# Optimization experiments

Measured on AMD Instinct MI355X. Metric: run time of the kernel, lower is better.

## Reference

```python
import jax, jax.numpy as jnp
import numpy as np

B = 128
N_ATOMS = 4096
NB, NA, NT = 4095, 4094, 4093
MAX_LEN = 5 * NT  # 20465, longest packed column (torsions)
EPS = 1e-8


def setup_inputs() -> dict:
    key = jax.random.key(0)
    ks = jax.random.split(key, 24)
    feats = jnp.zeros((B, MAX_LEN, 9), jnp.float32)
    # col 0: atom type ids
    atoms = jax.random.randint(ks[0], (B, N_ATOMS), 0, 6)
    # col 5: coords, flattened (N_ATOMS, 3)
    coords = jax.random.normal(ks[1], (B, N_ATOMS, 3), jnp.float32) * 5.0
    # col 6: bonds (i, j, type)
    bonds = jnp.stack([
        jax.random.randint(ks[2], (B, NB), 0, N_ATOMS),
        jax.random.randint(ks[3], (B, NB), 0, N_ATOMS),
        jax.random.randint(ks[4], (B, NB), 0, 15)], axis=-1)
    # col 7: angles (i, j, k, type)
    angles = jnp.stack([
        jax.random.randint(ks[5], (B, NA), 0, N_ATOMS),
        jax.random.randint(ks[6], (B, NA), 0, N_ATOMS),
        jax.random.randint(ks[7], (B, NA), 0, N_ATOMS),
        jax.random.randint(ks[8], (B, NA), 0, 13)], axis=-1)
    # col 8: torsions (i, j, k, l, type)
    tors = jnp.stack([
        jax.random.randint(ks[9], (B, NT), 0, N_ATOMS),
        jax.random.randint(ks[10], (B, NT), 0, N_ATOMS),
        jax.random.randint(ks[11], (B, NT), 0, N_ATOMS),
        jax.random.randint(ks[12], (B, NT), 0, N_ATOMS),
        jax.random.randint(ks[13], (B, NT), 0, 25)], axis=-1)
    feats = feats.at[:, :N_ATOMS, 0].set(atoms.astype(jnp.float32))
    feats = feats.at[:, :3 * N_ATOMS, 5].set(coords.reshape(B, -1))
    feats = feats.at[:, :3 * NB, 6].set(bonds.reshape(B, -1).astype(jnp.float32))
    feats = feats.at[:, :4 * NA, 7].set(angles.reshape(B, -1).astype(jnp.float32))
    feats = feats.at[:, :5 * NT, 8].set(tors.reshape(B, -1).astype(jnp.float32))
    lengths = jnp.tile(jnp.array(
        [[N_ATOMS, 0, 0, 0, 0, 3 * N_ATOMS, 3 * NB, 4 * NA, 5 * NT]],
        jnp.int32), (B, 1))
    bond_type = jnp.stack([jnp.ones(15), jax.random.uniform(ks[14], (15,), minval=1.0, maxval=2.0)], -1).astype(jnp.float32)
    angle_type = jnp.stack([jnp.ones(13), jax.random.uniform(ks[15], (13,), minval=1.0, maxval=3.0)], -1).astype(jnp.float32)
    tor_type = jnp.stack([jnp.ones(25), jax.random.uniform(ks[16], (25,), minval=0.0, maxval=3.14)], -1).astype(jnp.float32)
    multiplicity = jax.random.randint(ks[17], (25,), 1, 4)
    opt_pars = jax.random.uniform(ks[18], (47,), minval=0.5, maxval=1.5).astype(jnp.float32)
    return {"features": feats, "lengths": lengths, "bond_type": bond_type,
            "angle_type": angle_type, "tor_type": tor_type,
            "multiplicity": multiplicity, "opt_pars": opt_pars}


def _sample_energy(f, bond_type, angle_type, tor_type, multiplicity, opt_pars):
    coords = f[:3 * N_ATOMS, 5].reshape(-1, 3)                      # [N,3]
    bonds = f[:3 * NB, 6].astype(jnp.int32).reshape(-1, 3)          # [NB,3]
    angles = f[:4 * NA, 7].astype(jnp.int32).reshape(-1, 4)         # [NA,4]
    tors = f[:5 * NT, 8].astype(jnp.int32).reshape(-1, 5)           # [NT,5]

    # bonds: harmonic k*(r - r0)^2
    d = coords[bonds[:, 0]] - coords[bonds[:, 1]]
    r = jnp.sqrt(jnp.sum(d * d, -1) + EPS)
    pb = bond_type[bonds[:, 2]]
    e_bond = opt_pars[0] * jnp.sum(pb[:, 0] * (r - pb[:, 1]) ** 2)

    # angles: harmonic k*(theta - theta0)^2
    v1 = coords[angles[:, 0]] - coords[angles[:, 1]]
    v2 = coords[angles[:, 2]] - coords[angles[:, 1]]
    cosang = jnp.sum(v1 * v2, -1) / (
        jnp.sqrt(jnp.sum(v1 * v1, -1) + EPS) * jnp.sqrt(jnp.sum(v2 * v2, -1) + EPS))
    theta = jnp.arccos(jnp.clip(cosang, -1.0 + 1e-6, 1.0 - 1e-6))
    pa = angle_type[angles[:, 3]]
    e_ang = opt_pars[1] * jnp.sum(pa[:, 0] * (theta - pa[:, 1]) ** 2)

    # torsions: periodic k*(1 + cos(n*phi - delta))
    ci, cj, ck, cl = (coords[tors[:, m]] for m in range(4))
    b1, b2, b3 = cj - ci, ck - cj, cl - ck
    n1 = jnp.cross(b1, b2)
    n2 = jnp.cross(b2, b3)
    b2n = b2 / jnp.sqrt(jnp.sum(b2 * b2, -1, keepdims=True) + EPS)
    m1 = jnp.cross(n1, b2n)
    phi = jnp.arctan2(jnp.sum(m1 * n2, -1), jnp.sum(n1 * n2, -1))
    pt = tor_type[tors[:, 4]]
    n_mult = multiplicity[tors[:, 4]].astype(jnp.float32)
    e_tor = opt_pars[2] * jnp.sum(pt[:, 0] * (1.0 + jnp.cos(n_mult * phi - pt[:, 1])))

    return jnp.stack([e_bond, e_ang, e_tor])


def reference(features, lengths, bond_type, angle_type, tor_type, multiplicity, opt_pars):
    # lengths are uniform across batch (constants above); vmap over batch dim
    return jax.vmap(_sample_energy, in_axes=(0, None, None, None, None, None))(
        features, bond_type, angle_type, tor_type, multiplicity, opt_pars)
```

## Files before the change

kernel.cpp:

```cpp
#include <hip/hip_runtime.h>
#include <math.h>

#define BATCH      128
#define N_ATOMS    4096
#define NB         4095
#define NA         4094
#define NT         4093
#define FSTRIDE    184185
#define COORD_SPAN 110592
#define TOTAL_F4   5893920u
#define EPSV       1e-8f
#define THREADS    1024
#define WAVES      16
#define TILE_F     1080
#define NTILES     171
#define CTILES     103
#define SCR_F4     272

#define WAVE_LDS_FENCE()  do { asm volatile("" ::: "memory"); \
                               __builtin_amdgcn_wave_barrier(); } while (0)

__global__ __launch_bounds__(THREADS, 1) void
local_energy_fused(const float* __restrict__ F,
                   const float* __restrict__ bond_type,
                   const float* __restrict__ angle_type,
                   const float* __restrict__ tor_type,
                   const int*   __restrict__ multiplicity,
                   const float* __restrict__ opt_pars,
                   float*       __restrict__ out)
{
    __shared__ float scx[N_ATOMS];
    __shared__ float scy[N_ATOMS];
    __shared__ float scz[N_ATOMS];
    __shared__ __align__(16) float4 scr[WAVES][SCR_F4];
    __shared__ float sbt[30], sat[26], stt[50], smu[25];
    __shared__ float sred[WAVES * 3];

    const int b   = blockIdx.x;
    const int x   = b & 7;
    const int g   = b >> 3;
    const int s   = (g & 15) * 8 + x;
    const int p   = g >> 4;
    const int tid = threadIdx.x;
    const int w   = tid >> 6;
    const int l   = tid & 63;
    const size_t sbase = (size_t)s * FSTRIDE;
    const int d = (int)(sbase & 3);
    const float4* __restrict__ F4 = (const float4*)F;

    if (tid < 30)                      sbt[tid]       = bond_type[tid];
    else if (tid >= 32 && tid < 58)    sat[tid - 32]  = angle_type[tid - 32];
    else if (tid >= 64 && tid < 114)   stt[tid - 64]  = tor_type[tid - 64];
    else if (tid >= 128 && tid < 153)  smu[tid - 128] = (float)multiplicity[tid - 128];

    float* const swf = (float*)scr[w];

    {
        float4 cur[5];
        int t = w;
        {
            const size_t q0 = (sbase + (size_t)t * TILE_F) >> 2;
            const int nf = (COORD_SPAN - t * TILE_F < TILE_F) ? COORD_SPAN - t * TILE_F : TILE_F;
            const int nq = (d + nf + 3) >> 2;
            #pragma unroll
            for (int i = 0; i < 5; ++i) {
                const int k = l + 64 * i;
                cur[i] = (k < nq && q0 + k < TOTAL_F4) ? F4[q0 + k]
                                                       : make_float4(0.f, 0.f, 0.f, 0.f);
            }
        }
        for (; t < CTILES; t += WAVES) {
            const int tn = t + WAVES;
            float4 nxt[5];
            #pragma unroll
            for (int i = 0; i < 5; ++i) nxt[i] = make_float4(0.f, 0.f, 0.f, 0.f);
            if (tn < CTILES) {
                const size_t q0 = (sbase + (size_t)tn * TILE_F) >> 2;
                const int nf = (COORD_SPAN - tn * TILE_F < TILE_F) ? COORD_SPAN - tn * TILE_F : TILE_F;
                const int nq = (d + nf + 3) >> 2;
                #pragma unroll
                for (int i = 0; i < 5; ++i) {
                    const int k = l + 64 * i;
                    if (k < nq && q0 + k < TOTAL_F4) nxt[i] = F4[q0 + k];
                }
            }
            #pragma unroll
            for (int i = 0; i < 4; ++i) scr[w][l + 64 * i] = cur[i];
            if (l < 15) scr[w][l + 256] = cur[4];
            WAVE_LDS_FENCE();

            const int na = (N_ATOMS - 40 * t < 40) ? N_ATOMS - 40 * t : 40;
            if (l < na) {
                const int base = d + 27 * l;
                const int atom = 40 * t + l;
                scx[atom] = swf[base + 5];
                scy[atom] = swf[base + 14];
                scz[atom] = swf[base + 23];
            }
            WAVE_LDS_FENCE();
            #pragma unroll
            for (int i = 0; i < 5; ++i) cur[i] = nxt[i];
        }
    }
    __syncthreads();

    float e_bond = 0.f, e_ang = 0.f, e_tor = 0.f;
    {
        const int tlo = (p == 0) ? 0  : 86;
        const int thi = (p == 0) ? 86 : NTILES;
        float4 cur[5];
        int t = tlo + w;
        if (t < thi) {
            const size_t q0 = (sbase + (size_t)t * TILE_F) >> 2;
            const int nf = (FSTRIDE - t * TILE_F < TILE_F) ? FSTRIDE - t * TILE_F : TILE_F;
            const int nq = (d + nf + 3) >> 2;
            #pragma unroll
            for (int i = 0; i < 5; ++i) {
                const int k = l + 64 * i;
                cur[i] = (k < nq && q0 + k < TOTAL_F4) ? F4[q0 + k]
                                                       : make_float4(0.f, 0.f, 0.f, 0.f);
            }
        }
        for (; t < thi; t += WAVES) {
            const int tn = t + WAVES;
            float4 nxt[5];
            #pragma unroll
            for (int i = 0; i < 5; ++i) nxt[i] = make_float4(0.f, 0.f, 0.f, 0.f);
            if (tn < thi) {
                const size_t q0 = (sbase + (size_t)tn * TILE_F) >> 2;
                const int nf = (FSTRIDE - tn * TILE_F < TILE_F) ? FSTRIDE - tn * TILE_F : TILE_F;
                const int nq = (d + nf + 3) >> 2;
                #pragma unroll
                for (int i = 0; i < 5; ++i) {
                    const int k = l + 64 * i;
                    if (k < nq && q0 + k < TOTAL_F4) nxt[i] = F4[q0 + k];
                }
            }
            #pragma unroll
            for (int i = 0; i < 4; ++i) scr[w][l + 64 * i] = cur[i];
            if (l < 15) scr[w][l + 256] = cur[4];
            WAVE_LDS_FENCE();

            int nb = NB - 40 * t; nb = (nb > 40) ? 40 : nb;
            if (l < nb) {
                const int base = d + 27 * l;
                const int a0 = (int)swf[base + 6];
                const int a1 = (int)swf[base + 15];
                const int bt = (int)swf[base + 24];
                const float dx = scx[a0] - scx[a1];
                const float dy = scy[a0] - scy[a1];
                const float dz = scz[a0] - scz[a1];
                const float r  = sqrtf(dx*dx + dy*dy + dz*dz + EPSV);
                const float t0 = r - sbt[bt * 2 + 1];
                e_bond += sbt[bt * 2 + 0] * t0 * t0;
            }

            int na = NA - 30 * t; na = (na > 30) ? 30 : na;
            if (l < na) {
                const int base = d + 36 * l;
                const int a0 = (int)swf[base + 7];
                const int a1 = (int)swf[base + 16];
                const int a2 = (int)swf[base + 25];
                const int at = (int)swf[base + 34];
                const float v1x = scx[a0] - scx[a1];
                const float v1y = scy[a0] - scy[a1];
                const float v1z = scz[a0] - scz[a1];
                const float v2x = scx[a2] - scx[a1];
                const float v2y = scy[a2] - scy[a1];
                const float v2z = scz[a2] - scz[a1];
                const float d12 = v1x*v2x + v1y*v2y + v1z*v2z;
                const float n1  = sqrtf(v1x*v1x + v1y*v1y + v1z*v1z + EPSV);
                const float n2  = sqrtf(v2x*v2x + v2y*v2y + v2z*v2z + EPSV);
                float cosang = d12 / (n1 * n2);
                cosang = fminf(fmaxf(cosang, -1.0f + 1e-6f), 1.0f - 1e-6f);
                const float t0 = acosf(cosang) - sat[at * 2 + 1];
                e_ang += sat[at * 2 + 0] * t0 * t0;
            }

            int ntr = NT - 24 * t; ntr = (ntr > 24) ? 24 : ntr;
            if (l < ntr) {
                const int base = d + 45 * l;
                const int ai = (int)swf[base + 8];
                const int aj = (int)swf[base + 17];
                const int ak = (int)swf[base + 26];
                const int al = (int)swf[base + 35];
                const int tt = (int)swf[base + 44];

                const float b1x = scx[aj] - scx[ai], b1y = scy[aj] - scy[ai], b1z = scz[aj] - scz[ai];
                const float b2x = scx[ak] - scx[aj], b2y = scy[ak] - scy[aj], b2z = scz[ak] - scz[aj];
                const float b3x = scx[al] - scx[ak], b3y = scy[al] - scy[ak], b3z = scz[al] - scz[ak];

                const float n1x = b1y*b2z - b1z*b2y;
                const float n1y = b1z*b2x - b1x*b2z;
                const float n1z = b1x*b2y - b1y*b2x;
                const float n2x = b2y*b3z - b2z*b3y;
                const float n2y = b2z*b3x - b2x*b3z;
                const float n2z = b2x*b3y - b2y*b3x;

                const float inv = 1.0f / sqrtf(b2x*b2x + b2y*b2y + b2z*b2z + EPSV);
                const float bnx = b2x * inv, bny = b2y * inv, bnz = b2z * inv;

                const float m1x = n1y*bnz - n1z*bny;
                const float m1y = n1z*bnx - n1x*bnz;
                const float m1z = n1x*bny - n1y*bnx;

                const float sy = m1x*n2x + m1y*n2y + m1z*n2z;
                const float sx = n1x*n2x + n1y*n2y + n1z*n2z;
                const float phi = atan2f(sy, sx);

                e_tor += stt[tt * 2 + 0] * (1.0f + cosf(smu[tt] * phi - stt[tt * 2 + 1]));
            }

            WAVE_LDS_FENCE();
            #pragma unroll
            for (int i = 0; i < 5; ++i) cur[i] = nxt[i];
        }
    }

    for (int off = 32; off > 0; off >>= 1) {
        e_bond += __shfl_down(e_bond, off);
        e_ang  += __shfl_down(e_ang,  off);
        e_tor  += __shfl_down(e_tor,  off);
    }
    if (l == 0) {
        sred[w * 3 + 0] = e_bond;
        sred[w * 3 + 1] = e_ang;
        sred[w * 3 + 2] = e_tor;
    }
    __syncthreads();
    if (tid == 0) {
        float eb = 0.f, ea = 0.f, et = 0.f;
        for (int i = 0; i < WAVES; ++i) {
            eb += sred[i * 3 + 0];
            ea += sred[i * 3 + 1];
            et += sred[i * 3 + 2];
        }
        atomicAdd(&out[s * 3 + 0], opt_pars[0] * eb);
        atomicAdd(&out[s * 3 + 1], opt_pars[1] * ea);
        atomicAdd(&out[s * 3 + 2], opt_pars[2] * et);
    }
}

extern "C" void kernel_launch(void* const* d_in, const int* in_sizes, int n_in,
                              void* d_out, int out_size, void* d_ws, size_t ws_size,
                              hipStream_t stream) {
    const float* F            = (const float*)d_in[0];
    const float* bond_type    = (const float*)d_in[2];
    const float* angle_type   = (const float*)d_in[3];
    const float* tor_type     = (const float*)d_in[4];
    const int*   multiplicity = (const int*)  d_in[5];
    const float* opt_pars     = (const float*)d_in[6];
    float* out = (float*)d_out;

    hipMemsetAsync(out, 0, (size_t)out_size * sizeof(float), stream);

    local_energy_fused<<<dim3(BATCH * 2), dim3(THREADS), 0, stream>>>(
        F, bond_type, angle_type, tor_type, multiplicity, opt_pars, out);
}
```

Baseline: 158.3 us.

## Stash bond/angle/torsion indices in LDS during coord pass to balance work

During the coordinate-loading pass (tiles 0-102), each block now also decodes the bond, angle and torsion index records in its half of that range into compact ushort arrays in LDS. It evaluates them afterwards with all threads in flat strided loops. The second streaming pass now covers only tiles 103-170, which hold the remaining angles and torsions. This avoids re-reading tiles that are already in cache, splits the work evenly across the two blocks per sample, and removes bounds checks. In exchange it uses more LDS and adds a second compute phase whose gathers may have more bank conflicts.

```diff
diff --git a/kernel.cpp b/kernel.cpp
--- a/kernel.cpp
+++ b/kernel.cpp
@@ -7,14 +7,13 @@
 #define NA         4094
 #define NT         4093
 #define FSTRIDE    184185
-#define COORD_SPAN 110592
 #define TOTAL_F4   5893920u
 #define EPSV       1e-8f
 #define THREADS    1024
 #define WAVES      16
 #define TILE_F     1080
 #define NTILES     171
-#define CTILES     103
+#define ATILES     103
 #define SCR_F4     272
 
 #define WAVE_LDS_FENCE()  do { asm volatile("" ::: "memory"); \
@@ -33,6 +32,9 @@
     __shared__ float scy[N_ATOMS];
     __shared__ float scz[N_ATOMS];
     __shared__ __align__(16) float4 scr[WAVES][SCR_F4];
+    __shared__ unsigned short sbB[2080 * 3];
+    __shared__ unsigned short sbA[1560 * 4];
+    __shared__ unsigned short sbT[1248 * 5];
     __shared__ float sbt[30], sat[26], stt[50], smu[25];
     __shared__ float sred[WAVES * 3];
 
@@ -55,33 +57,35 @@
 
     float* const swf = (float*)scr[w];
 
+    const int Alo = p ? 51 : 0;
+    const int Ahi = p ? 103 : 51;
+    const int cnt_b = p ? 2055 : 2040;
+    const int cnt_a = p ? 1560 : 1530;
+    const int cnt_t = p ? 1248 : 1224;
+
     {
+        const int nq = (d + TILE_F + 3) >> 2;
         float4 cur[5];
         int t = w;
         {
             const size_t q0 = (sbase + (size_t)t * TILE_F) >> 2;
-            const int nf = (COORD_SPAN - t * TILE_F < TILE_F) ? COORD_SPAN - t * TILE_F : TILE_F;
-            const int nq = (d + nf + 3) >> 2;
             #pragma unroll
             for (int i = 0; i < 5; ++i) {
                 const int k = l + 64 * i;
-                cur[i] = (k < nq && q0 + k < TOTAL_F4) ? F4[q0 + k]
-                                                       : make_float4(0.f, 0.f, 0.f, 0.f);
-            }
-        }
-        for (; t < CTILES; t += WAVES) {
+                cur[i] = (k < nq) ? F4[q0 + k] : make_float4(0.f, 0.f, 0.f, 0.f);
+            }
+        }
+        for (; t < ATILES; t += WAVES) {
             const int tn = t + WAVES;
             float4 nxt[5];
             #pragma unroll
             for (int i = 0; i < 5; ++i) nxt[i] = make_float4(0.f, 0.f, 0.f, 0.f);
-            if (tn < CTILES) {
+            if (tn < ATILES) {
                 const size_t q0 = (sbase + (size_t)tn * TILE_F) >> 2;
-                const int nf = (COORD_SPAN - tn * TILE_F < TILE_F) ? COORD_SPAN - tn * TILE_F : TILE_F;
-                const int nq = (d + nf + 3) >> 2;
                 #pragma unroll
                 for (int i = 0; i < 5; ++i) {
                     const int k = l + 64 * i;
-                    if (k < nq && q0 + k < TOTAL_F4) nxt[i] = F4[q0 + k];
+                    if (k < nq) nxt[i] = F4[q0 + k];
                 }
             }
             #pragma unroll
@@ -97,6 +101,34 @@
                 scy[atom] = swf[base + 14];
                 scz[atom] = swf[base + 23];
             }
+            if (t >= Alo && t < Ahi) {
+                const int lt = t - Alo;
+                int nb = NB - 40 * t; nb = (nb > 40) ? 40 : nb;
+                if (l < nb) {
+                    const int sl = (lt * 40 + l) * 3;
+                    const int base = d + 27 * l;
+                    sbB[sl + 0] = (unsigned short)(int)swf[base + 6];
+                    sbB[sl + 1] = (unsigned short)(int)swf[base + 15];
+                    sbB[sl + 2] = (unsigned short)(int)swf[base + 24];
+                }
+                if (l < 30) {
+                    const int sl = (lt * 30 + l) * 4;
+                    const int base = d + 36 * l;
+                    sbA[sl + 0] = (unsigned short)(int)swf[base + 7];
+                    sbA[sl + 1] = (unsigned short)(int)swf[base + 16];
+                    sbA[sl + 2] = (unsigned short)(int)swf[base + 25];
+                    sbA[sl + 3] = (unsigned short)(int)swf[base + 34];
+                }
+                if (l < 24) {
+                    const int sl = (lt * 24 + l) * 5;
+                    const int base = d + 45 * l;
+                    sbT[sl + 0] = (unsigned short)(int)swf[base + 8];
+                    sbT[sl + 1] = (unsigned short)(int)swf[base + 17];
+                    sbT[sl + 2] = (unsigned short)(int)swf[base + 26];
+                    sbT[sl + 3] = (unsigned short)(int)swf[base + 35];
+                    sbT[sl + 4] = (unsigned short)(int)swf[base + 44];
+                }
+            }
             WAVE_LDS_FENCE();
             #pragma unroll
             for (int i = 0; i < 5; ++i) cur[i] = nxt[i];
@@ -105,12 +137,13 @@
     __syncthreads();
 
     float e_bond = 0.f, e_ang = 0.f, e_tor = 0.f;
+
     {
-        const int tlo = (p == 0) ? 0  : 86;
-        const int thi = (p == 0) ? 86 : NTILES;
+        const int tlo = p ? 137 : 103;
+        const int thi = p ? 171 : 137;
         float4 cur[5];
         int t = tlo + w;
-        if (t < thi) {
+        {
             const size_t q0 = (sbase + (size_t)t * TILE_F) >> 2;
             const int nf = (FSTRIDE - t * TILE_F < TILE_F) ? FSTRIDE - t * TILE_F : TILE_F;
             const int nq = (d + nf + 3) >> 2;
@@ -140,20 +173,6 @@
             for (int i = 0; i < 4; ++i) scr[w][l + 64 * i] = cur[i];
             if (l < 15) scr[w][l + 256] = cur[4];
             WAVE_LDS_FENCE();
-
-            int nb = NB - 40 * t; nb = (nb > 40) ? 40 : nb;
-            if (l < nb) {
-                const int base = d + 27 * l;
-                const int a0 = (int)swf[base + 6];
-                const int a1 = (int)swf[base + 15];
-                const int bt = (int)swf[base + 24];
-                const float dx = scx[a0] - scx[a1];
-                const float dy = scy[a0] - scy[a1];
-                const float dz = scz[a0] - scz[a1];
-                const float r  = sqrtf(dx*dx + dy*dy + dz*dz + EPSV);
-                const float t0 = r - sbt[bt * 2 + 1];
-                e_bond += sbt[bt * 2 + 0] * t0 * t0;
-            }
 
             int na = NA - 30 * t; na = (na > 30) ? 30 : na;
             if (l < na) {
@@ -185,29 +204,22 @@
                 const int ak = (int)swf[base + 26];
                 const int al = (int)swf[base + 35];
                 const int tt = (int)swf[base + 44];
-
                 const float b1x = scx[aj] - scx[ai], b1y = scy[aj] - scy[ai], b1z = scz[aj] - scz[ai];
                 const float b2x = scx[ak] - scx[aj], b2y = scy[ak] - scy[aj], b2z = scz[ak] - scz[aj];
                 const float b3x = scx[al] - scx[ak], b3y = scy[al] - scy[ak], b3z = scz[al] - scz[ak];
-
                 const float n1x = b1y*b2z - b1z*b2y;
                 const float n1y = b1z*b2x - b1x*b2z;
                 const float n1z = b1x*b2y - b1y*b2x;
                 const float n2x = b2y*b3z - b2z*b3y;
                 const float n2y = b2z*b3x - b2x*b3z;
                 const float n2z = b2x*b3y - b2y*b3x;
-
                 const float inv = 1.0f / sqrtf(b2x*b2x + b2y*b2y + b2z*b2z + EPSV);
                 const float bnx = b2x * inv, bny = b2y * inv, bnz = b2z * inv;
-
                 const float m1x = n1y*bnz - n1z*bny;
                 const float m1y = n1z*bnx - n1x*bnz;
                 const float m1z = n1x*bny - n1y*bnx;
-
-                const float sy = m1x*n2x + m1y*n2y + m1z*n2z;
-                const float sx = n1x*n2x + n1y*n2y + n1z*n2z;
-                const float phi = atan2f(sy, sx);
-
+                const float phi = atan2f(m1x*n2x + m1y*n2y + m1z*n2z,
+                                         n1x*n2x + n1y*n2y + n1z*n2z);
                 e_tor += stt[tt * 2 + 0] * (1.0f + cosf(smu[tt] * phi - stt[tt * 2 + 1]));
             }
 
@@ -215,6 +227,61 @@
             #pragma unroll
             for (int i = 0; i < 5; ++i) cur[i] = nxt[i];
         }
+    }
+
+    for (int i = tid; i < cnt_b; i += THREADS) {
+        const int a0 = sbB[3 * i + 0];
+        const int a1 = sbB[3 * i + 1];
+        const int bt = sbB[3 * i + 2];
+        const float dx = scx[a0] - scx[a1];
+        const float dy = scy[a0] - scy[a1];
+        const float dz = scz[a0] - scz[a1];
+        const float r  = sqrtf(dx*dx + dy*dy + dz*dz + EPSV);
+        const float t0 = r - sbt[bt * 2 + 1];
+        e_bond += sbt[bt * 2 + 0] * t0 * t0;
+    }
+    for (int i = tid; i < cnt_a; i += THREADS) {
+        const int a0 = sbA[4 * i + 0];
+        const int a1 = sbA[4 * i + 1];
+        const int a2 = sbA[4 * i + 2];
+        const int at = sbA[4 * i + 3];
+        const float v1x = scx[a0] - scx[a1];
+        const float v1y = scy[a0] - scy[a1];
+        const float v1z = scz[a0] - scz[a1];
+        const float v2x = scx[a2] - scx[a1];
+        const float v2y = scy[a2] - scy[a1];
+        const float v2z = scz[a2] - scz[a1];
+        const float d12 = v1x*v2x + v1y*v2y + v1z*v2z;
+        const float n1  = sqrtf(v1x*v1x + v1y*v1y + v1z*v1z + EPSV);
+        const float n2  = sqrtf(v2x*v2x + v2y*v2y + v2z*v2z + EPSV);
+        float cosang = d12 / (n1 * n2);
+        cosang = fminf(fmaxf(cosang, -1.0f + 1e-6f), 1.0f - 1e-6f);
+        const float t0 = acosf(cosang) - sat[at * 2 + 1];
+        e_ang += sat[at * 2 + 0] * t0 * t0;
+    }
+    for (int i = tid; i < cnt_t; i += THREADS) {
+        const int ai = sbT[5 * i + 0];
+        const int aj = sbT[5 * i + 1];
+        const int ak = sbT[5 * i + 2];
+        const int al = sbT[5 * i + 3];
+        const int tt = sbT[5 * i + 4];
+        const float b1x = scx[aj] - scx[ai], b1y = scy[aj] - scy[ai], b1z = scz[aj] - scz[ai];
+        const float b2x = scx[ak] - scx[aj], b2y = scy[ak] - scy[aj], b2z = scz[ak] - scz[aj];
+        const float b3x = scx[al] - scx[ak], b3y = scy[al] - scy[ak], b3z = scz[al] - scz[ak];
+        const float n1x = b1y*b2z - b1z*b2y;
+        const float n1y = b1z*b2x - b1x*b2z;
+        const float n1z = b1x*b2y - b1y*b2x;
+        const float n2x = b2y*b3z - b2z*b3y;
+        const float n2y = b2z*b3x - b2x*b3z;
+        const float n2z = b2x*b3y - b2y*b3x;
+        const float inv = 1.0f / sqrtf(b2x*b2x + b2y*b2y + b2z*b2z + EPSV);
+        const float bnx = b2x * inv, bny = b2y * inv, bnz = b2z * inv;
+        const float m1x = n1y*bnz - n1z*bny;
+        const float m1y = n1z*bnx - n1x*bnz;
+        const float m1z = n1x*bny - n1y*bnx;
+        const float phi = atan2f(m1x*n2x + m1y*n2y + m1z*n2z,
+                                 n1x*n2x + n1y*n2y + n1z*n2z);
+        e_tor += stt[tt * 2 + 0] * (1.0f + cosf(smu[tt] * phi - stt[tt * 2 + 1]));
     }
 
     for (int off = 32; off > 0; off >>= 1) {
```

After: 159.0 us. Within noise of the previous version (+0.4%).

## Split into extract kernel writing compact SoA workspace and energy kernel

Applied to the files above, without the earlier changes.

Replaces the single fused kernel with two kernels. The first streams the strided feature tensor once across 512 blocks and writes planar coordinates plus packed 16-bit index records to a workspace. The second loads the coordinates into LDS and computes the bond, angle and torsion energies from the compact records. This removes the re-reading of the coordinate span by both half-blocks and the per-wave tile decode in the compute path. In exchange it adds a second launch and a workspace write/read round trip, and it depends on ws_size being large enough.

```diff
diff --git a/kernel.cpp b/kernel.cpp
--- a/kernel.cpp
+++ b/kernel.cpp
@@ -7,34 +7,28 @@
 #define NA         4094
 #define NT         4093
 #define FSTRIDE    184185
-#define COORD_SPAN 110592
 #define TOTAL_F4   5893920u
 #define EPSV       1e-8f
-#define THREADS    1024
-#define WAVES      16
 #define TILE_F     1080
 #define NTILES     171
-#define CTILES     103
 #define SCR_F4     272
+
+#define PLANE      (BATCH * N_ATOMS)
+#define WS_CX      0
+#define WS_CY      PLANE
+#define WS_CZ      (2 * PLANE)
+#define WS_BND_B   ((size_t)3 * PLANE * 4)
+#define WS_ANG_B   (WS_BND_B + (size_t)BATCH * 4096 * 8)
+#define WS_TOR_B   (WS_ANG_B + (size_t)BATCH * 4096 * 8)
+#define WS_END_B   (WS_TOR_B + (size_t)BATCH * 4096 * 16)
 
 #define WAVE_LDS_FENCE()  do { asm volatile("" ::: "memory"); \
                                __builtin_amdgcn_wave_barrier(); } while (0)
 
-__global__ __launch_bounds__(THREADS, 1) void
-local_energy_fused(const float* __restrict__ F,
-                   const float* __restrict__ bond_type,
-                   const float* __restrict__ angle_type,
-                   const float* __restrict__ tor_type,
-                   const int*   __restrict__ multiplicity,
-                   const float* __restrict__ opt_pars,
-                   float*       __restrict__ out)
+__global__ __launch_bounds__(512, 1) void
+extract_kernel(const float* __restrict__ F, float* __restrict__ ws)
 {
-    __shared__ float scx[N_ATOMS];
-    __shared__ float scy[N_ATOMS];
-    __shared__ float scz[N_ATOMS];
-    __shared__ __align__(16) float4 scr[WAVES][SCR_F4];
-    __shared__ float sbt[30], sat[26], stt[50], smu[25];
-    __shared__ float sred[WAVES * 3];
+    __shared__ __align__(16) float4 scr[8][SCR_F4];
 
     const int b   = blockIdx.x;
     const int x   = b & 7;
@@ -48,172 +42,202 @@
     const int d = (int)(sbase & 3);
     const float4* __restrict__ F4 = (const float4*)F;
 
+    float* __restrict__ cx = ws + WS_CX + (size_t)s * N_ATOMS;
+    float* __restrict__ cy = ws + WS_CY + (size_t)s * N_ATOMS;
+    float* __restrict__ cz = ws + WS_CZ + (size_t)s * N_ATOMS;
+    ushort4* __restrict__ bw = (ushort4*)((char*)ws + WS_BND_B) + (size_t)s * 4096;
+    ushort4* __restrict__ aw = (ushort4*)((char*)ws + WS_ANG_B) + (size_t)s * 4096;
+    uint4*   __restrict__ tw = (uint4*)  ((char*)ws + WS_TOR_B) + (size_t)s * 4096;
+
+    const int tlo = p * 43;
+    const int thi = (tlo + 43 < NTILES) ? tlo + 43 : NTILES;
+    float* const swf = (float*)scr[w];
+
+    float4 cur[5];
+    int t = tlo + w;
+    if (t < thi) {
+        const size_t q0 = (sbase + (size_t)t * TILE_F) >> 2;
+        const int nf = (FSTRIDE - t * TILE_F < TILE_F) ? FSTRIDE - t * TILE_F : TILE_F;
+        const int nq = (d + nf + 3) >> 2;
+        #pragma unroll
+        for (int i = 0; i < 5; ++i) {
+            const int k = l + 64 * i;
+            cur[i] = (k < nq && q0 + k < TOTAL_F4) ? F4[q0 + k]
+                                                   : make_float4(0.f, 0.f, 0.f, 0.f);
+        }
+    }
+    for (; t < thi; t += 8) {
+        const int tn = t + 8;
+        float4 nxt[5];
+        #pragma unroll
+        for (int i = 0; i < 5; ++i) nxt[i] = make_float4(0.f, 0.f, 0.f, 0.f);
+        if (tn < thi) {
+            const size_t q0 = (sbase + (size_t)tn * TILE_F) >> 2;
+            const int nf = (FSTRIDE - tn * TILE_F < TILE_F) ? FSTRIDE - tn * TILE_F : TILE_F;
+            const int nq = (d + nf + 3) >> 2;
+            #pragma unroll
+            for (int i = 0; i < 5; ++i) {
+                const int k = l + 64 * i;
+                if (k < nq && q0 + k < TOTAL_F4) nxt[i] = F4[q0 + k];
+            }
+        }
+        #pragma unroll
+        for (int i = 0; i < 4; ++i) scr[w][l + 64 * i] = cur[i];
+        if (l < 15) scr[w][l + 256] = cur[4];
+        WAVE_LDS_FENCE();
+
+        int nat = N_ATOMS - 40 * t; nat = (nat > 40) ? 40 : nat;
+        if (l < nat) {
+            const int base = d + 27 * l;
+            const int a = 40 * t + l;
+            cx[a] = swf[base + 5];
+            cy[a] = swf[base + 14];
+            cz[a] = swf[base + 23];
+        }
+        int nb = NB - 40 * t; nb = (nb > 40) ? 40 : nb;
+        if (l < nb) {
+            const int base = d + 27 * l;
+            ushort4 r;
+            r.x = (unsigned short)(int)swf[base + 6];
+            r.y = (unsigned short)(int)swf[base + 15];
+            r.z = (unsigned short)(int)swf[base + 24];
+            r.w = 0;
+            bw[40 * t + l] = r;
+        }
+        int na = NA - 30 * t; na = (na > 30) ? 30 : na;
+        if (l < na) {
+            const int base = d + 36 * l;
+            ushort4 r;
+            r.x = (unsigned short)(int)swf[base + 7];
+            r.y = (unsigned short)(int)swf[base + 16];
+            r.z = (unsigned short)(int)swf[base + 25];
+            r.w = (unsigned short)(int)swf[base + 34];
+            aw[30 * t + l] = r;
+        }
+        int ntr = NT - 24 * t; ntr = (ntr > 24) ? 24 : ntr;
+        if (l < ntr) {
+            const int base = d + 45 * l;
+            uint4 r;
+            r.x = (unsigned)(unsigned short)(int)swf[base + 8]
+                | ((unsigned)(unsigned short)(int)swf[base + 17] << 16);
+            r.y = (unsigned)(unsigned short)(int)swf[base + 26]
+                | ((unsigned)(unsigned short)(int)swf[base + 35] << 16);
+            r.z = (unsigned)(unsigned short)(int)swf[base + 44];
+            r.w = 0;
+            tw[24 * t + l] = r;
+        }
+        WAVE_LDS_FENCE();
+        #pragma unroll
+        for (int i = 0; i < 5; ++i) cur[i] = nxt[i];
+    }
+}
+
+#define THREADS 1024
+__global__ __launch_bounds__(THREADS, 1) void
+energy_kernel(const float* __restrict__ ws,
+              const float* __restrict__ bond_type,
+              const float* __restrict__ angle_type,
+              const float* __restrict__ tor_type,
+              const int*   __restrict__ multiplicity,
+              const float* __restrict__ opt_pars,
+              float*       __restrict__ out)
+{
+    __shared__ float scx[N_ATOMS];
+    __shared__ float scy[N_ATOMS];
+    __shared__ float scz[N_ATOMS];
+    __shared__ float sbt[30], sat[26], stt[50], smu[25];
+    __shared__ float sred[16 * 3];
+
+    const int b   = blockIdx.x;
+    const int x   = b & 7;
+    const int g   = b >> 3;
+    const int s   = (g & 15) * 8 + x;
+    const int p   = g >> 4;
+    const int tid = threadIdx.x;
+    const int w   = tid >> 6;
+    const int l   = tid & 63;
+
     if (tid < 30)                      sbt[tid]       = bond_type[tid];
     else if (tid >= 32 && tid < 58)    sat[tid - 32]  = angle_type[tid - 32];
     else if (tid >= 64 && tid < 114)   stt[tid - 64]  = tor_type[tid - 64];
     else if (tid >= 128 && tid < 153)  smu[tid - 128] = (float)multiplicity[tid - 128];
 
-    float* const swf = (float*)scr[w];
-
-    {
-        float4 cur[5];
-        int t = w;
-        {
-            const size_t q0 = (sbase + (size_t)t * TILE_F) >> 2;
-            const int nf = (COORD_SPAN - t * TILE_F < TILE_F) ? COORD_SPAN - t * TILE_F : TILE_F;
-            const int nq = (d + nf + 3) >> 2;
-            #pragma unroll
-            for (int i = 0; i < 5; ++i) {
-                const int k = l + 64 * i;
-                cur[i] = (k < nq && q0 + k < TOTAL_F4) ? F4[q0 + k]
-                                                       : make_float4(0.f, 0.f, 0.f, 0.f);
-            }
-        }
-        for (; t < CTILES; t += WAVES) {
-            const int tn = t + WAVES;
-            float4 nxt[5];
-            #pragma unroll
-            for (int i = 0; i < 5; ++i) nxt[i] = make_float4(0.f, 0.f, 0.f, 0.f);
-            if (tn < CTILES) {
-                const size_t q0 = (sbase + (size_t)tn * TILE_F) >> 2;
-                const int nf = (COORD_SPAN - tn * TILE_F < TILE_F) ? COORD_SPAN - tn * TILE_F : TILE_F;
-                const int nq = (d + nf + 3) >> 2;
-                #pragma unroll
-                for (int i = 0; i < 5; ++i) {
-                    const int k = l + 64 * i;
-                    if (k < nq && q0 + k < TOTAL_F4) nxt[i] = F4[q0 + k];
-                }
-            }
-            #pragma unroll
-            for (int i = 0; i < 4; ++i) scr[w][l + 64 * i] = cur[i];
-            if (l < 15) scr[w][l + 256] = cur[4];
-            WAVE_LDS_FENCE();
-
-            const int na = (N_ATOMS - 40 * t < 40) ? N_ATOMS - 40 * t : 40;
-            if (l < na) {
-                const int base = d + 27 * l;
-                const int atom = 40 * t + l;
-                scx[atom] = swf[base + 5];
-                scy[atom] = swf[base + 14];
-                scz[atom] = swf[base + 23];
-            }
-            WAVE_LDS_FENCE();
-            #pragma unroll
-            for (int i = 0; i < 5; ++i) cur[i] = nxt[i];
-        }
+    {
+        const float4* __restrict__ cx4 = (const float4*)(ws + WS_CX + (size_t)s * N_ATOMS);
+        const float4* __restrict__ cy4 = (const float4*)(ws + WS_CY + (size_t)s * N_ATOMS);
+        const float4* __restrict__ cz4 = (const float4*)(ws + WS_CZ + (size_t)s * N_ATOMS);
+        ((float4*)scx)[tid] = cx4[tid];
+        ((float4*)scy)[tid] = cy4[tid];
+        ((float4*)scz)[tid] = cz4[tid];
     }
     __syncthreads();
 
     float e_bond = 0.f, e_ang = 0.f, e_tor = 0.f;
-    {
-        const int tlo = (p == 0) ? 0  : 86;
-        const int thi = (p == 0) ? 86 : NTILES;
-        float4 cur[5];
-        int t = tlo + w;
-        if (t < thi) {
-            const size_t q0 = (sbase + (size_t)t * TILE_F) >> 2;
-            const int nf = (FSTRIDE - t * TILE_F < TILE_F) ? FSTRIDE - t * TILE_F : TILE_F;
-            const int nq = (d + nf + 3) >> 2;
-            #pragma unroll
-            for (int i = 0; i < 5; ++i) {
-                const int k = l + 64 * i;
-                cur[i] = (k < nq && q0 + k < TOTAL_F4) ? F4[q0 + k]
-                                                       : make_float4(0.f, 0.f, 0.f, 0.f);
-            }
-        }
-        for (; t < thi; t += WAVES) {
-            const int tn = t + WAVES;
-            float4 nxt[5];
-            #pragma unroll
-            for (int i = 0; i < 5; ++i) nxt[i] = make_float4(0.f, 0.f, 0.f, 0.f);
-            if (tn < thi) {
-                const size_t q0 = (sbase + (size_t)tn * TILE_F) >> 2;
-                const int nf = (FSTRIDE - tn * TILE_F < TILE_F) ? FSTRIDE - tn * TILE_F : TILE_F;
-                const int nq = (d + nf + 3) >> 2;
-                #pragma unroll
-                for (int i = 0; i < 5; ++i) {
-                    const int k = l + 64 * i;
-                    if (k < nq && q0 + k < TOTAL_F4) nxt[i] = F4[q0 + k];
-                }
-            }
-            #pragma unroll
-            for (int i = 0; i < 4; ++i) scr[w][l + 64 * i] = cur[i];
-            if (l < 15) scr[w][l + 256] = cur[4];
-            WAVE_LDS_FENCE();
-
-            int nb = NB - 40 * t; nb = (nb > 40) ? 40 : nb;
-            if (l < nb) {
-                const int base = d + 27 * l;
-                const int a0 = (int)swf[base + 6];
-                const int a1 = (int)swf[base + 15];
-                const int bt = (int)swf[base + 24];
-                const float dx = scx[a0] - scx[a1];
-                const float dy = scy[a0] - scy[a1];
-                const float dz = scz[a0] - scz[a1];
-                const float r  = sqrtf(dx*dx + dy*dy + dz*dz + EPSV);
-                const float t0 = r - sbt[bt * 2 + 1];
-                e_bond += sbt[bt * 2 + 0] * t0 * t0;
-            }
-
-            int na = NA - 30 * t; na = (na > 30) ? 30 : na;
-            if (l < na) {
-                const int base = d + 36 * l;
-                const int a0 = (int)swf[base + 7];
-                const int a1 = (int)swf[base + 16];
-                const int a2 = (int)swf[base + 25];
-                const int at = (int)swf[base + 34];
-                const float v1x = scx[a0] - scx[a1];
-                const float v1y = scy[a0] - scy[a1];
-                const float v1z = scz[a0] - scz[a1];
-                const float v2x = scx[a2] - scx[a1];
-                const float v2y = scy[a2] - scy[a1];
-                const float v2z = scz[a2] - scz[a1];
-                const float d12 = v1x*v2x + v1y*v2y + v1z*v2z;
-                const float n1  = sqrtf(v1x*v1x + v1y*v1y + v1z*v1z + EPSV);
-                const float n2  = sqrtf(v2x*v2x + v2y*v2y + v2z*v2z + EPSV);
-                float cosang = d12 / (n1 * n2);
-                cosang = fminf(fmaxf(cosang, -1.0f + 1e-6f), 1.0f - 1e-6f);
-                const float t0 = acosf(cosang) - sat[at * 2 + 1];
-                e_ang += sat[at * 2 + 0] * t0 * t0;
-            }
-
-            int ntr = NT - 24 * t; ntr = (ntr > 24) ? 24 : ntr;
-            if (l < ntr) {
-                const int base = d + 45 * l;
-                const int ai = (int)swf[base + 8];
-                const int aj = (int)swf[base + 17];
-                const int ak = (int)swf[base + 26];
-                const int al = (int)swf[base + 35];
-                const int tt = (int)swf[base + 44];
-
-                const float b1x = scx[aj] - scx[ai], b1y = scy[aj] - scy[ai], b1z = scz[aj] - scz[ai];
-                const float b2x = scx[ak] - scx[aj], b2y = scy[ak] - scy[aj], b2z = scz[ak] - scz[aj];
-                const float b3x = scx[al] - scx[ak], b3y = scy[al] - scy[ak], b3z = scz[al] - scz[ak];
-
-                const float n1x = b1y*b2z - b1z*b2y;
-                const float n1y = b1z*b2x - b1x*b2z;
-                const float n1z = b1x*b2y - b1y*b2x;
-                const float n2x = b2y*b3z - b2z*b3y;
-                const float n2y = b2z*b3x - b2x*b3z;
-                const float n2z = b2x*b3y - b2y*b3x;
-
-                const float inv = 1.0f / sqrtf(b2x*b2x + b2y*b2y + b2z*b2z + EPSV);
-                const float bnx = b2x * inv, bny = b2y * inv, bnz = b2z * inv;
-
-                const float m1x = n1y*bnz - n1z*bny;
-                const float m1y = n1z*bnx - n1x*bnz;
-                const float m1z = n1x*bny - n1y*bnx;
-
-                const float sy = m1x*n2x + m1y*n2y + m1z*n2z;
-                const float sx = n1x*n2x + n1y*n2y + n1z*n2z;
-                const float phi = atan2f(sy, sx);
-
-                e_tor += stt[tt * 2 + 0] * (1.0f + cosf(smu[tt] * phi - stt[tt * 2 + 1]));
-            }
-
-            WAVE_LDS_FENCE();
-            #pragma unroll
-            for (int i = 0; i < 5; ++i) cur[i] = nxt[i];
+    const int lo = p * 2048;
+
+    {
+        const ushort4* __restrict__ bp =
+            (const ushort4*)((const char*)ws + WS_BND_B) + (size_t)s * 4096;
+        const int hi = (lo + 2048 < NB) ? lo + 2048 : NB;
+        for (int i = lo + tid; i < hi; i += THREADS) {
+            const ushort4 u = bp[i];
+            const int a0 = u.x, a1 = u.y, bt = u.z;
+            const float dx = scx[a0] - scx[a1];
+            const float dy = scy[a0] - scy[a1];
+            const float dz = scz[a0] - scz[a1];
+            const float r  = sqrtf(dx*dx + dy*dy + dz*dz + EPSV);
+            const float t0 = r - sbt[bt * 2 + 1];
+            e_bond += sbt[bt * 2 + 0] * t0 * t0;
+        }
+    }
+    {
+        const ushort4* __restrict__ ap =
+            (const ushort4*)((const char*)ws + WS_ANG_B) + (size_t)s * 4096;
+        const int hi = (lo + 2048 < NA) ? lo + 2048 : NA;
+        for (int i = lo + tid; i < hi; i += THREADS) {
+            const ushort4 u = ap[i];
+            const int a0 = u.x, a1 = u.y, a2 = u.z, at = u.w;
+            const float v1x = scx[a0] - scx[a1];
+            const float v1y = scy[a0] - scy[a1];
+            const float v1z = scz[a0] - scz[a1];
+            const float v2x = scx[a2] - scx[a1];
+            const float v2y = scy[a2] - scy[a1];
+            const float v2z = scz[a2] - scz[a1];
+            const float d12 = v1x*v2x + v1y*v2y + v1z*v2z;
+            const float n1  = sqrtf(v1x*v1x + v1y*v1y + v1z*v1z + EPSV);
+            const float n2  = sqrtf(v2x*v2x + v2y*v2y + v2z*v2z + EPSV);
+            float cosang = d12 / (n1 * n2);
+            cosang = fminf(fmaxf(cosang, -1.0f + 1e-6f), 1.0f - 1e-6f);
+            const float t0 = acosf(cosang) - sat[at * 2 + 1];
+            e_ang += sat[at * 2 + 0] * t0 * t0;
+        }
+    }
+    {
+        const uint4* __restrict__ tp =
+            (const uint4*)((const char*)ws + WS_TOR_B) + (size_t)s * 4096;
+        const int hi = (lo + 2048 < NT) ? lo + 2048 : NT;
+        for (int i = lo + tid; i < hi; i += THREADS) {
+            const uint4 u = tp[i];
+            const int ai = u.x & 0xFFFF, aj = u.x >> 16;
+            const int ak = u.y & 0xFFFF, al = u.y >> 16;
+            const int tt = u.z & 0xFFFF;
+            const float b1x = scx[aj] - scx[ai], b1y = scy[aj] - scy[ai], b1z = scz[aj] - scz[ai];
+            const float b2x = scx[ak] - scx[aj], b2y = scy[ak] - scy[aj], b2z = scz[ak] - scz[aj];
+            const float b3x = scx[al] - scx[ak], b3y = scy[al] - scy[ak], b3z = scz[al] - scz[ak];
+            const float n1x = b1y*b2z - b1z*b2y;
+            const float n1y = b1z*b2x - b1x*b2z;
+            const float n1z = b1x*b2y - b1y*b2x;
+            const float n2x = b2y*b3z - b2z*b3y;
+            const float n2y = b2z*b3x - b2x*b3z;
+            const float n2z = b2x*b3y - b2y*b3x;
+            const float inv = 1.0f / sqrtf(b2x*b2x + b2y*b2y + b2z*b2z + EPSV);
+            const float bnx = b2x * inv, bny = b2y * inv, bnz = b2z * inv;
+            const float m1x = n1y*bnz - n1z*bny;
+            const float m1y = n1z*bnx - n1x*bnz;
+            const float m1z = n1x*bny - n1y*bnx;
+            const float phi = atan2f(m1x*n2x + m1y*n2y + m1z*n2z,
+                                     n1x*n2x + n1y*n2y + n1z*n2z);
+            e_tor += stt[tt * 2 + 0] * (1.0f + cosf(smu[tt] * phi - stt[tt * 2 + 1]));
         }
     }
 
@@ -230,7 +254,7 @@
     __syncthreads();
     if (tid == 0) {
         float eb = 0.f, ea = 0.f, et = 0.f;
-        for (int i = 0; i < WAVES; ++i) {
+        for (int i = 0; i < 16; ++i) {
             eb += sred[i * 3 + 0];
             ea += sred[i * 3 + 1];
             et += sred[i * 3 + 2];
@@ -251,9 +275,11 @@
     const int*   multiplicity = (const int*)  d_in[5];
     const float* opt_pars     = (const float*)d_in[6];
     float* out = (float*)d_out;
+    float* ws  = (float*)d_ws;
 
     hipMemsetAsync(out, 0, (size_t)out_size * sizeof(float), stream);
 
-    local_energy_fused<<<dim3(BATCH * 2), dim3(THREADS), 0, stream>>>(
-        F, bond_type, angle_type, tor_type, multiplicity, opt_pars, out);
+    extract_kernel<<<dim3(512), dim3(512), 0, stream>>>(F, ws);
+    energy_kernel<<<dim3(256), dim3(THREADS), 0, stream>>>(
+        ws, bond_type, angle_type, tor_type, multiplicity, opt_pars, out);
 }
```

Result: slower. 163.6 us (+3.3%).
